# Kernel tuning notes

Measured on AMD Instinct MI355X. Metric: run time of the kernel, lower is better.

## Reference

```python
import jax, jax.numpy as jnp
import numpy as np
from jax import lax

NER_PAD_ID = 0


def _crf_log_likelihood(emissions, labels, mask, start_transitions, end_transitions, transitions):
    # emissions: [B,T,L], labels: [B,T] int, mask: [B,T] bool (mask[:,0] must be True)
    B, T, L = emissions.shape
    dt = emissions.dtype
    # ---- numerator: score of the gold path ----
    em_tag = jnp.take_along_axis(emissions, labels[..., None], axis=2)[..., 0]  # [B,T]
    score = start_transitions[labels[:, 0]] + em_tag[:, 0]
    trans_score = transitions[labels[:, :-1], labels[:, 1:]]                    # [B,T-1]
    m = mask[:, 1:].astype(dt)
    score = score + jnp.sum(m * (trans_score + em_tag[:, 1:]), axis=1)
    last_idx = jnp.sum(mask.astype(jnp.int32), axis=1) - 1                      # [B]
    last_tag = jnp.take_along_axis(labels, last_idx[:, None], axis=1)[:, 0]
    score = score + end_transitions[last_tag]
    # ---- denominator: log partition via forward algorithm (scan over time) ----
    em_t = jnp.transpose(emissions, (1, 0, 2))   # [T,B,L]
    mask_t = jnp.transpose(mask, (1, 0))          # [T,B]
    alpha0 = start_transitions[None, :] + em_t[0]  # [B,L]

    def fwd_step(alpha, x):
        em, mk = x  # em [B,L], mk [B]
        nxt = jax.nn.logsumexp(alpha[:, :, None] + transitions[None, :, :], axis=1) + em
        alpha = jnp.where(mk[:, None], nxt, alpha)
        return alpha, None

    alpha, _ = lax.scan(fwd_step, alpha0, (em_t[1:], mask_t[1:]))
    log_z = jax.nn.logsumexp(alpha + end_transitions[None, :], axis=-1)  # [B]
    return score - log_z


def _viterbi_decode(emissions, mask, start_transitions, end_transitions, transitions,
                    label_pad_token_id=NER_PAD_ID):
    B, T, L = emissions.shape
    em_t = jnp.transpose(emissions, (1, 0, 2))   # [T,B,L]
    mask_t = jnp.transpose(mask, (1, 0))          # [T,B]
    score0 = start_transitions[None, :] + em_t[0]
    ident = jnp.arange(L, dtype=jnp.int32)[None, :]

    def vit_step(score, x):
        em, mk = x
        br = score[:, :, None] + transitions[None, :, :]      # [B,L_prev,L_next]
        best = jnp.max(br, axis=1) + em                        # [B,L]
        idx = jnp.argmax(br, axis=1).astype(jnp.int32)         # [B,L]
        new_score = jnp.where(mk[:, None], best, score)
        bp = jnp.where(mk[:, None], idx, ident)                # identity backptr when masked
        return new_score, bp

    final_score, history = lax.scan(vit_step, score0, (em_t[1:], mask_t[1:]))  # history [T-1,B,L]
    last_tag = jnp.argmax(final_score + end_transitions[None, :], axis=-1).astype(jnp.int32)  # [B]

    def back_step(tag, bp):
        prev = jnp.take_along_axis(bp, tag[:, None], axis=1)[:, 0]
        return prev, prev

    _, tags_rev = lax.scan(back_step, last_tag, history, reverse=True)  # [T-1,B] tags for pos 0..T-2
    tags = jnp.concatenate([jnp.transpose(tags_rev, (1, 0)), last_tag[:, None]], axis=1)  # [B,T]
    return jnp.where(mask, tags, jnp.int32(label_pad_token_id)).astype(jnp.int64)


def setup_inputs() -> dict:
    key = jax.random.key(0)
    ks = jax.random.split(key, 6)
    B, T, H, L = 128, 512, 1024, 23
    hidden_states = jax.random.normal(ks[0], (B, T, H), jnp.float32)
    attention_mask = jnp.ones((B, T), jnp.int32)
    labels = jax.random.randint(ks[1], (B, T), 0, L, dtype=jnp.int32).astype(jnp.int64)
    W = jax.random.normal(ks[2], (H, L), jnp.float32) / np.float32(np.sqrt(H))
    b = jnp.zeros((L,), jnp.float32)
    start_transitions = 0.1 * jax.random.normal(ks[3], (L,), jnp.float32)
    end_transitions = 0.1 * jax.random.normal(ks[4], (L,), jnp.float32)
    transitions = 0.1 * jax.random.normal(ks[5], (L, L), jnp.float32)
    return {"hidden_states": hidden_states, "attention_mask": attention_mask,
            "labels": labels, "W": W, "b": b,
            "start_transitions": start_transitions,
            "end_transitions": end_transitions, "transitions": transitions}


def reference(hidden_states, attention_mask, labels, W, b,
              start_transitions, end_transitions, transitions):
    mask = attention_mask == 1
    # dropout is identity at eval time
    emissions = jnp.einsum('bth,hl->btl', hidden_states, W) + b  # [B,T,L]
    llh = _crf_log_likelihood(emissions, labels, mask,
                              start_transitions, end_transitions, transitions)
    loss = -jnp.mean(llh)  # reduction='mean', loss = -logits
    pred_labels = _viterbi_decode(emissions, mask,
                                  start_transitions, end_transitions, transitions)
    return loss, pred_labels
```

## Files before the change

kernel.cpp:

```cpp
#include <hip/hip_runtime.h>
#include <hip/hip_bf16.h>
#include <math.h>

#define B_ 128
#define T_ 512
#define H_ 1024
#define L_ 23
#define EMS 24
#define NINF (-1.0f/0.0f)

__device__ __forceinline__ float rdl(float v, int l) {
  return __int_as_float(__builtin_amdgcn_readlane(__float_as_int(v), l));
}
__device__ __forceinline__ float rdfl(float v) {
  return __int_as_float(__builtin_amdgcn_readfirstlane(__float_as_int(v)));
}

#define EK 64
#define ES 67
__global__ __launch_bounds__(256) void emis_kernel(
    const float* __restrict__ hs, const float* __restrict__ W,
    const float* __restrict__ bias, float* __restrict__ em) {
  __shared__ float tile[2][64 * ES];
  const int tid = threadIdx.x;
  const int rowbase = blockIdx.x * 64;
  const int r = tid & 63;
  const int q = tid >> 6;
  const int lr = tid >> 4;
  const int lc = tid & 15;
  const float* gsrc = hs + (size_t)(rowbase + lr) * H_ + lc * 4;

  float4 st[4];
#define LOADC(c)                                                        \
  { _Pragma("unroll") for (int m = 0; m < 4; ++m)                       \
      st[m] = *(const float4*)(gsrc + (size_t)(16 * m) * H_ + (c)*EK); }
#define WRITEC(buf)                                                     \
  { _Pragma("unroll") for (int m = 0; m < 4; ++m) {                     \
      float* p = &tile[buf][(lr + 16 * m) * ES + lc * 4];               \
      p[0] = st[m].x; p[1] = st[m].y; p[2] = st[m].z; p[3] = st[m].w; } }

  float acc[L_];
#pragma unroll
  for (int l = 0; l < L_; ++l) acc[l] = 0.f;

  LOADC(0); WRITEC(0); LOADC(1);
  __syncthreads();

  for (int c = 0; c < 16; ++c) {
    const float* tp = &tile[c & 1][r * ES + q * 16];
    const float* wk = W + (size_t)(c * EK + q * 16) * L_;
#pragma unroll
    for (int kk = 0; kk < 16; ++kk) {
      float x = tp[kk];
      const float* wr = wk + kk * L_;
#pragma unroll
      for (int l = 0; l < L_; ++l) acc[l] = fmaf(x, wr[l], acc[l]);
    }
    if (c < 15) {
      WRITEC((c + 1) & 1);
      if (c < 14) LOADC(c + 2);
      __syncthreads();
    }
  }

  __syncthreads();
  float* comb = (float*)tile;
  if (q > 0) {
    float* p = comb + ((q - 1) * 64 + r) * L_;
#pragma unroll
    for (int l = 0; l < L_; ++l) p[l] = acc[l];
  }
  __syncthreads();
  if (q == 0) {
#pragma unroll
    for (int l = 0; l < L_; ++l)
      acc[l] = acc[l] + comb[(0 * 64 + r) * L_ + l] + comb[(1 * 64 + r) * L_ + l]
             + comb[(2 * 64 + r) * L_ + l] + bias[l];
    float4* op = (float4*)(em + (size_t)(rowbase + r) * EMS);
    op[0] = make_float4(acc[0], acc[1], acc[2], acc[3]);
    op[1] = make_float4(acc[4], acc[5], acc[6], acc[7]);
    op[2] = make_float4(acc[8], acc[9], acc[10], acc[11]);
    op[3] = make_float4(acc[12], acc[13], acc[14], acc[15]);
    op[4] = make_float4(acc[16], acc[17], acc[18], acc[19]);
    op[5] = make_float4(acc[20], acc[21], acc[22], 0.0f);
  }
}

__global__ __launch_bounds__(128) void crf_kernel(
    const float* __restrict__ em, const int* __restrict__ am,
    const int* __restrict__ labels, const float* __restrict__ startT,
    const float* __restrict__ endT, const float* __restrict__ trans,
    float* __restrict__ llh, float* __restrict__ out) {
  __shared__ float emb_lds[2][64 * EMS];
  __shared__ int bp_lds[(T_ - 1) * L_];
  __shared__ int tags_sh[T_];
  __shared__ float score_sh;

  const int role = blockIdx.x & 1;
  const int b = blockIdx.x >> 1;
  const int wid = threadIdx.x >> 6;
  const int lane = threadIdx.x & 63;
  const int eml = (lane < L_) ? lane : 0;
  const float* emb = em + (size_t)b * T_ * EMS;
  const int* amb = am + b * T_;
  const int* lab = labels + b * T_;

  float state = NINF;
  float colT[L_];
  float st_r = 0.f, end_r = 0.f;
  if (wid == 0) {
    st_r = startT[eml];
    end_r = endT[eml];
#pragma unroll
    for (int i = 0; i < L_; ++i) {
      float tv = trans[i * L_ + eml];
      colT[i] = (role == 0) ? __expf(tv) : tv;
    }
  }

  int av = amb[lane];

  for (int c = 0; c < 8; ++c) {
    if (wid == 1) {
      const float* src = emb + c * (64 * EMS);
      float4 v[6];
#pragma unroll
      for (int i = 0; i < 6; ++i)
        v[i] = *(const float4*)(src + i * 256 + lane * 4);
#pragma unroll
      for (int i = 0; i < 6; ++i)
        *(float4*)&emb_lds[c & 1][i * 256 + lane * 4] = v[i];
    }
    __syncthreads();
    if (wid == 0) {
      int av_nxt = (c < 7) ? amb[(c + 1) * 64 + lane] : 0;
      unsigned long long mkb = __ballot(av == 1);
      const float* eb = &emb_lds[c & 1][0];
      int s0 = 0;
      if (c == 0) {
        state = (lane < L_) ? st_r + eb[lane] : NINF;
        s0 = 1;
      }
      if (role == 0) {
#pragma unroll 4
        for (int s = s0; s < 64; ++s) {
          float ee = eb[s * EMS + eml];
          bool mk = (mkb >> s) & 1ull;
          float m0 = rdfl(state);
          float ex = __expf(state - m0);
          float p0 = 0.f, p1 = 0.f, p2 = 0.f, p3 = 0.f;
#pragma unroll
          for (int i = 0; i < 20; i += 4) {
            p0 = fmaf(rdl(ex, i + 0), colT[i + 0], p0);
            p1 = fmaf(rdl(ex, i + 1), colT[i + 1], p1);
            p2 = fmaf(rdl(ex, i + 2), colT[i + 2], p2);
            p3 = fmaf(rdl(ex, i + 3), colT[i + 3], p3);
          }
          p0 = fmaf(rdl(ex, 20), colT[20], p0);
          p1 = fmaf(rdl(ex, 21), colT[21], p1);
          p2 = fmaf(rdl(ex, 22), colT[22], p2);
          float sum = (p0 + p1) + (p2 + p3);
          float nxt = m0 + __logf(sum) + ee;
          state = (mk && lane < L_) ? nxt : state;
        }
      } else {
#pragma unroll 2
        for (int s = s0; s < 64; ++s) {
          int t = c * 64 + s;
          float ee = eb[s * EMS + eml];
          bool mk = (mkb >> s) & 1ull;
          float ci[L_];
#pragma unroll
          for (int i = 0; i < L_; ++i) ci[i] = rdl(state, i) + colT[i];
          float m1[12];
#pragma unroll
          for (int i = 0; i < 11; ++i) m1[i] = fmaxf(ci[2 * i], ci[2 * i + 1]);
          m1[11] = ci[22];
          float m2[6];
#pragma unroll
          for (int i = 0; i < 6; ++i) m2[i] = fmaxf(m1[2 * i], m1[2 * i + 1]);
          float m3a = fmaxf(m2[0], m2[1]), m3b = fmaxf(m2[2], m2[3]),
                m3c = fmaxf(m2[4], m2[5]);
          float best = fmaxf(fmaxf(m3a, m3b), m3c);
          int bi = 22;
#pragma unroll
          for (int i = 21; i >= 0; --i) bi = (ci[i] == best) ? i : bi;
          float snew = best + ee;
          int bpv = mk ? bi : lane;
          state = (mk && lane < L_) ? snew : state;
          if (lane < L_) bp_lds[(t - 1) * L_ + lane] = bpv;
        }
      }
      av = av_nxt;
    }
  }

  if (wid == 1 && role == 0) {
    float sc = 0.f;
    int cnt = 0;
#pragma unroll
    for (int it = 0; it < 8; ++it) {
      int t = it * 64 + lane;
      int mk = (amb[t] == 1);
      cnt += mk;
      int lt = lab[t];
      float emt = emb[t * EMS + lt];
      if (t == 0) sc += startT[lt] + emt;
      else if (mk) sc += trans[lab[t - 1] * L_ + lt] + emt;
    }
#pragma unroll
    for (int off = 32; off >= 1; off >>= 1) {
      sc += __shfl_xor(sc, off);
      cnt += __shfl_xor(cnt, off);
    }
    sc += endT[lab[cnt - 1]];
    if (lane == 0) score_sh = sc;
  }
  __syncthreads();

  if (wid == 0) {
    if (role == 0) {
      float v = (lane < L_) ? state + end_r : NINF;
      float mx = v;
#pragma unroll
      for (int off = 32; off >= 1; off >>= 1) mx = fmaxf(mx, __shfl_xor(mx, off));
      float e2 = __expf(v - mx);
#pragma unroll
      for (int off = 32; off >= 1; off >>= 1) e2 += __shfl_xor(e2, off);
      if (lane == 0) llh[b] = score_sh - (mx + __logf(e2));
    } else {
      float v = (lane < L_) ? state + end_r : NINF;
      float mx = v;
#pragma unroll
      for (int off = 32; off >= 1; off >>= 1) mx = fmaxf(mx, __shfl_xor(mx, off));
      int cand = (v == mx && lane < L_) ? lane : 64;
#pragma unroll
      for (int off = 32; off >= 1; off >>= 1) cand = min(cand, __shfl_xor(cand, off));
      int cur = __builtin_amdgcn_readfirstlane(cand);
      if (lane == 0) tags_sh[T_ - 1] = cur;
#pragma unroll 8
      for (int t = T_ - 2; t >= 0; --t) {
        int row = bp_lds[t * L_ + eml];
        cur = __builtin_amdgcn_readlane(row, cur);
        if (lane == 0) tags_sh[t] = cur;
      }
      for (int t = lane; t < T_; t += 64) {
        float o = (amb[t] == 1) ? (float)tags_sh[t] : 0.0f;
        out[1 + b * T_ + t] = o;
      }
    }
  }
}

__global__ void finalize_kernel(const float* __restrict__ llh,
                                float* __restrict__ out) {
  int lane = threadIdx.x;
  float v = llh[lane] + llh[lane + 64];
#pragma unroll
  for (int off = 32; off >= 1; off >>= 1) v += __shfl_xor(v, off);
  if (lane == 0) out[0] = -v * (1.0f / (float)B_);
}

extern "C" void kernel_launch(void* const* d_in, const int* in_sizes, int n_in,
                              void* d_out, int out_size, void* d_ws, size_t ws_size,
                              hipStream_t stream) {
  const float* hs     = (const float*)d_in[0];
  const int*   am     = (const int*)d_in[1];
  const int*   labels = (const int*)d_in[2];
  const float* W      = (const float*)d_in[3];
  const float* bias   = (const float*)d_in[4];
  const float* startT = (const float*)d_in[5];
  const float* endT   = (const float*)d_in[6];
  const float* trans  = (const float*)d_in[7];
  float* out = (float*)d_out;

  float* em  = (float*)d_ws;
  float* llh = em + (size_t)B_ * T_ * EMS;

  emis_kernel<<<B_ * T_ / 64, 256, 0, stream>>>(hs, W, bias, em);
  crf_kernel<<<2 * B_, 128, 0, stream>>>(em, am, labels, startT, endT, trans, llh, out);
  finalize_kernel<<<1, 64, 0, stream>>>(llh, out);
}
```

Before: 749.2 us.

## Load hidden states directly into registers, dropping LDS staging in emission GEMV

The emission projection no longer stages hidden-state tiles through double-buffered shared memory. Each thread instead reads its own row's contiguous K-quarter as float4 vectors into registers, with register double buffering (va/vb), and the W row offset is made wave-uniform so it can use scalar loads. This removes LDS writes, reads and barriers from the main loop. The cost is less coalesced global access, since each lane strides by a full row, and higher register pressure.

Measured after the change: 762.4 us. About the same (+1.8%).

```diff
diff --git a/kernel.cpp b/kernel.cpp
--- a/kernel.cpp
+++ b/kernel.cpp
@@ -16,55 +16,59 @@
   return __int_as_float(__builtin_amdgcn_readfirstlane(__float_as_int(v)));
 }
 
-#define EK 64
-#define ES 67
 __global__ __launch_bounds__(256) void emis_kernel(
     const float* __restrict__ hs, const float* __restrict__ W,
     const float* __restrict__ bias, float* __restrict__ em) {
-  __shared__ float tile[2][64 * ES];
+  __shared__ float comb[3 * 64 * L_];
   const int tid = threadIdx.x;
-  const int rowbase = blockIdx.x * 64;
   const int r = tid & 63;
   const int q = tid >> 6;
-  const int lr = tid >> 4;
-  const int lc = tid & 15;
-  const float* gsrc = hs + (size_t)(rowbase + lr) * H_ + lc * 4;
-
-  float4 st[4];
-#define LOADC(c)                                                        \
-  { _Pragma("unroll") for (int m = 0; m < 4; ++m)                       \
-      st[m] = *(const float4*)(gsrc + (size_t)(16 * m) * H_ + (c)*EK); }
-#define WRITEC(buf)                                                     \
-  { _Pragma("unroll") for (int m = 0; m < 4; ++m) {                     \
-      float* p = &tile[buf][(lr + 16 * m) * ES + lc * 4];               \
-      p[0] = st[m].x; p[1] = st[m].y; p[2] = st[m].z; p[3] = st[m].w; } }
+  const int row = blockIdx.x * 64 + r;
+  const float4* x4 = (const float4*)(hs + (size_t)row * H_) + q * 64;
+  const float* Wq = W + (size_t)__builtin_amdgcn_readfirstlane(q * 256) * L_;
 
   float acc[L_];
 #pragma unroll
   for (int l = 0; l < L_; ++l) acc[l] = 0.f;
 
-  LOADC(0); WRITEC(0); LOADC(1);
-  __syncthreads();
-
-  for (int c = 0; c < 16; ++c) {
-    const float* tp = &tile[c & 1][r * ES + q * 16];
-    const float* wk = W + (size_t)(c * EK + q * 16) * L_;
-#pragma unroll
-    for (int kk = 0; kk < 16; ++kk) {
-      float x = tp[kk];
-      const float* wr = wk + kk * L_;
-#pragma unroll
-      for (int l = 0; l < L_; ++l) acc[l] = fmaf(x, wr[l], acc[l]);
-    }
-    if (c < 15) {
-      WRITEC((c + 1) & 1);
-      if (c < 14) LOADC(c + 2);
-      __syncthreads();
-    }
-  }
-
-  __syncthreads();
-  float* comb = (float*)tile;
+#define FMA4(vv, wb)                                                     \
+  { const float* wp = (wb);                                              \
+    _Pragma("unroll") for (int l = 0; l < L_; ++l)                       \
+      acc[l] = fmaf((vv).x, wp[l], acc[l]);                              \
+    _Pragma("unroll") for (int l = 0; l < L_; ++l)                       \
+      acc[l] = fmaf((vv).y, wp[L_ + l], acc[l]);                         \
+    _Pragma("unroll") for (int l = 0; l < L_; ++l)                       \
+      acc[l] = fmaf((vv).z, wp[2 * L_ + l], acc[l]);                     \
+    _Pragma("unroll") for (int l = 0; l < L_; ++l)                       \
+      acc[l] = fmaf((vv).w, wp[3 * L_ + l], acc[l]); }
+
+  float4 va[8], vb[8];
+#pragma unroll
+  for (int u = 0; u < 8; ++u) va[u] = x4[u];
+
+  for (int gp = 0; gp < 4; ++gp) {
+    {
+      const int g = 2 * gp;
+      if (g < 7) {
+#pragma unroll
+        for (int u = 0; u < 8; ++u) vb[u] = x4[(g + 1) * 8 + u];
+      }
+      const float* wg = Wq + (size_t)(g * 32) * L_;
+#pragma unroll
+      for (int u = 0; u < 8; ++u) FMA4(va[u], wg + (size_t)(u * 4) * L_);
+    }
+    {
+      const int g = 2 * gp + 1;
+      if (g < 7) {
+#pragma unroll
+        for (int u = 0; u < 8; ++u) va[u] = x4[(g + 1) * 8 + u];
+      }
+      const float* wg = Wq + (size_t)(g * 32) * L_;
+#pragma unroll
+      for (int u = 0; u < 8; ++u) FMA4(vb[u], wg + (size_t)(u * 4) * L_);
+    }
+  }
+
   if (q > 0) {
     float* p = comb + ((q - 1) * 64 + r) * L_;
 #pragma unroll
@@ -76,7 +80,7 @@
     for (int l = 0; l < L_; ++l)
       acc[l] = acc[l] + comb[(0 * 64 + r) * L_ + l] + comb[(1 * 64 + r) * L_ + l]
              + comb[(2 * 64 + r) * L_ + l] + bias[l];
-    float4* op = (float4*)(em + (size_t)(rowbase + r) * EMS);
+    float4* op = (float4*)(em + (size_t)row * EMS);
     op[0] = make_float4(acc[0], acc[1], acc[2], acc[3]);
     op[1] = make_float4(acc[4], acc[5], acc[6], acc[7]);
     op[2] = make_float4(acc[8], acc[9], acc[10], acc[11]);
```
